# Kernel optimization log

Measured on AMD Instinct MI355X. Metric: run time of the kernel, lower is better.

The kernel has to match this reference:

```python
import jax, jax.numpy as jnp
import numpy as np

N_NODES = 50000
N_EDGES = 800000
IN_DIM = 128
HIDDEN = 32
HEADS = 4
OUT_DIM = 40
NEG_SLOPE = 0.2


def _segment_softmax(logits, seg, num_segments):
    # logits: [E, H], seg: [E] destination node ids
    m = jax.ops.segment_max(logits, seg, num_segments=num_segments)  # [N, H]
    e = jnp.exp(logits - m[seg])
    s = jax.ops.segment_sum(e, seg, num_segments=num_segments)  # [N, H]
    return e / s[seg]


def _gat_conv(x, src, dst, W, a_src, a_dst, b, heads, out_ch, concat):
    N = x.shape[0]
    h = (x @ W).reshape(N, heads, out_ch)  # [N, H, C]
    alpha_src = jnp.einsum('nhc,hc->nh', h, a_src)  # [N, H]
    alpha_dst = jnp.einsum('nhc,hc->nh', h, a_dst)  # [N, H]
    logits = jax.nn.leaky_relu(alpha_src[src] + alpha_dst[dst], NEG_SLOPE)  # [E, H]
    alpha = _segment_softmax(logits, dst, N)  # [E, H]
    msg = h[src] * alpha[:, :, None]  # [E, H, C]
    out = jax.ops.segment_sum(msg, dst, num_segments=N)  # [N, H, C]
    if concat:
        out = out.reshape(N, heads * out_ch)
    else:
        out = out.mean(axis=1)
    return out + b


def setup_inputs() -> dict:
    key = jax.random.key(0)
    ks = jax.random.split(key, 12)
    x = jax.random.normal(ks[0], (N_NODES, IN_DIM), dtype=jnp.float32)
    edge_index = jax.random.randint(ks[1], (2, N_EDGES), 0, N_NODES, dtype=jnp.int64 if jax.config.read('jax_enable_x64') else jnp.int32)
    s1 = 1.0 / np.sqrt(IN_DIM)
    W1 = jax.random.uniform(ks[2], (IN_DIM, HEADS * HIDDEN), jnp.float32, -s1, s1)
    att_src1 = jax.random.uniform(ks[3], (HEADS, HIDDEN), jnp.float32, -1, 1) / np.sqrt(HIDDEN)
    att_dst1 = jax.random.uniform(ks[4], (HEADS, HIDDEN), jnp.float32, -1, 1) / np.sqrt(HIDDEN)
    b1 = jnp.zeros((HEADS * HIDDEN,), jnp.float32)
    s2 = 1.0 / np.sqrt(HEADS * HIDDEN)
    W2 = jax.random.uniform(ks[5], (HEADS * HIDDEN, OUT_DIM), jnp.float32, -s2, s2)
    att_src2 = jax.random.uniform(ks[6], (1, OUT_DIM), jnp.float32, -1, 1) / np.sqrt(OUT_DIM)
    att_dst2 = jax.random.uniform(ks[7], (1, OUT_DIM), jnp.float32, -1, 1) / np.sqrt(OUT_DIM)
    b2 = jnp.zeros((OUT_DIM,), jnp.float32)
    return {
        'x': x, 'edge_index': edge_index,
        'W1': W1, 'att_src1': att_src1, 'att_dst1': att_dst1, 'b1': b1,
        'W2': W2, 'att_src2': att_src2, 'att_dst2': att_dst2, 'b2': b2,
    }


def reference(x, edge_index, W1, att_src1, att_dst1, b1, W2, att_src2, att_dst2, b2):
    N = x.shape[0]
    # PyG GATConv default add_self_loops=True
    loop = jnp.arange(N, dtype=edge_index.dtype)
    src = jnp.concatenate([edge_index[0], loop])
    dst = jnp.concatenate([edge_index[1], loop])
    # dropout(p=0.6) is identity in eval mode
    h = _gat_conv(x, src, dst, W1, att_src1, att_dst1, b1, HEADS, HIDDEN, concat=True)
    h = jax.nn.relu(h)
    out = _gat_conv(h, src, dst, W2, att_src2, att_dst2, b2, 1, OUT_DIM, concat=True)
    return out
```

## Files before the change

### kernel.cpp

```cpp
#include <hip/hip_runtime.h>
#include <hip/hip_bf16.h>
#include <hip/hip_fp16.h>
#include <math.h>

#define N_NODES 50000
#define N_EDGES 800000
#define E_TOT   850000
#define IN_DIM  128
#define HID     32
#define HEADS   4
#define D1      128
#define OUT_DIM 40
#define H2P     64
#define NEG_SLOPE 0.2f
#define CAP     96

#define SCAN_TILE 1024
#define SCAN_NB   ((N_NODES + SCAN_TILE - 1) / SCAN_TILE)
#define GEMM1_NB  ((N_NODES + 63) / 64)
#define W2T_LD    132

typedef _Float16 f16x8 __attribute__((ext_vector_type(8)));
typedef float    f32x4 __attribute__((ext_vector_type(4)));

__global__ __launch_bounds__(256) void init_wf_deg(
    const float* __restrict__ W, _Float16* __restrict__ wf, int* __restrict__ deg)
{
  const int b = blockIdx.x, t = threadIdx.x;
  if (b < 64) {
    int tid = b * 256 + t;
    int j = tid & 7, lane = (tid >> 3) & 63, nt = (tid >> 9) & 7, kc = tid >> 12;
    int k = kc * 32 + ((lane >> 4) << 3) + j;
    int n = nt * 16 + (lane & 15);
    wf[tid] = (_Float16)W[k * D1 + n];
  } else {
    int i = (b - 64) * 256 + t;
    if (i < N_NODES) deg[i] = 0;
  }
}

__global__ __launch_bounds__(256) void gemm1_mfma_count(
    const float* __restrict__ x, const _Float16* __restrict__ wf,
    const float* __restrict__ as_v, const float* __restrict__ ad_v,
    _Float16* __restrict__ h1h, float* __restrict__ asrc, float* __restrict__ adst,
    const int* __restrict__ ei, int* __restrict__ deg)
{
  const int t = threadIdx.x;
  const int wave = t >> 6, lane = t & 63;
  const int lr = lane & 15, lq = lane >> 4;
  const int rowbase = blockIdx.x * 64 + wave * 16;
  const int arow = rowbase + lr;

  f32x4 acc[8];
#pragma unroll
  for (int nt = 0; nt < 8; ++nt) acc[nt] = (f32x4){0.f, 0.f, 0.f, 0.f};

  const float* xrow = x + (size_t)arow * IN_DIM;
  const f16x8* wfv = reinterpret_cast<const f16x8*>(wf);
#pragma unroll
  for (int kc = 0; kc < 4; ++kc) {
    float4 lo = make_float4(0.f, 0.f, 0.f, 0.f), hi = lo;
    if (arow < N_NODES) {
      lo = *reinterpret_cast<const float4*>(xrow + kc * 32 + lq * 8);
      hi = *reinterpret_cast<const float4*>(xrow + kc * 32 + lq * 8 + 4);
    }
    f16x8 a;
    a[0] = (_Float16)lo.x; a[1] = (_Float16)lo.y; a[2] = (_Float16)lo.z; a[3] = (_Float16)lo.w;
    a[4] = (_Float16)hi.x; a[5] = (_Float16)hi.y; a[6] = (_Float16)hi.z; a[7] = (_Float16)hi.w;
    const f16x8* bbase = wfv + (size_t)(kc * 8) * 64 + lane;
#pragma unroll
    for (int nt = 0; nt < 8; ++nt) {
      f16x8 bfrag = bbase[nt * 64];
      acc[nt] = __builtin_amdgcn_mfma_f32_16x16x32_f16(a, bfrag, acc[nt], 0, 0, 0);
    }
  }

  float as_lo[4], as_hi[4], ad_lo[4], ad_hi[4];
#pragma unroll
  for (int h = 0; h < 4; ++h) {
    as_lo[h] = as_v[h * HID + lr];      ad_lo[h] = ad_v[h * HID + lr];
    as_hi[h] = as_v[h * HID + 16 + lr]; ad_hi[h] = ad_v[h * HID + 16 + lr];
  }
#pragma unroll
  for (int nt = 0; nt < 8; ++nt) {
#pragma unroll
    for (int r = 0; r < 4; ++r) {
      int m = rowbase + lq * 4 + r;
      if (m < N_NODES) h1h[(size_t)m * D1 + nt * 16 + lr] = (_Float16)acc[nt][r];
    }
  }
#pragma unroll
  for (int h = 0; h < 4; ++h) {
#pragma unroll
    for (int r = 0; r < 4; ++r) {
      float ps = acc[2 * h][r] * as_lo[h] + acc[2 * h + 1][r] * as_hi[h];
      float pd = acc[2 * h][r] * ad_lo[h] + acc[2 * h + 1][r] * ad_hi[h];
#pragma unroll
      for (int off = 1; off < 16; off <<= 1) {
        ps += __shfl_xor(ps, off, 64);
        pd += __shfl_xor(pd, off, 64);
      }
      int m = rowbase + lq * 4 + r;
      if (lr == 0 && m < N_NODES) {
        asrc[m * HEADS + h] = ps;
        adst[m * HEADS + h] = pd;
      }
    }
  }
  for (int e = blockIdx.x * 256 + t; e < E_TOT; e += gridDim.x * 256) {
    int d = (e < N_EDGES) ? ei[N_EDGES + e] : e - N_EDGES;
    atomicAdd(deg + d, 1);
  }
}

__global__ __launch_bounds__(256) void scan_p1(const int* __restrict__ deg,
                                               int* __restrict__ blocksum)
{
  int base = blockIdx.x * SCAN_TILE + threadIdx.x * 4;
  int s = 0;
#pragma unroll
  for (int i = 0; i < 4; ++i) {
    int idx = base + i;
    if (idx < N_NODES) s += deg[idx];
  }
#pragma unroll
  for (int off = 1; off < 64; off <<= 1) s += __shfl_xor(s, off, 64);
  __shared__ int ws[4];
  if ((threadIdx.x & 63) == 0) ws[threadIdx.x >> 6] = s;
  __syncthreads();
  if (threadIdx.x == 0) blocksum[blockIdx.x] = ws[0] + ws[1] + ws[2] + ws[3];
}

__global__ void scan_p2(const int* __restrict__ blocksum, int* __restrict__ blockoff,
                        int* __restrict__ row_off)
{
  int t = threadIdx.x;
  int v = (t < SCAN_NB) ? blocksum[t] : 0;
  int incl = v;
#pragma unroll
  for (int off = 1; off < 64; off <<= 1) {
    int u = __shfl_up(incl, off, 64);
    if (t >= off) incl += u;
  }
  if (t < SCAN_NB) blockoff[t] = incl - v;
  if (t == 0) row_off[N_NODES] = E_TOT;
}

__global__ __launch_bounds__(256) void scan_p3(const int* __restrict__ deg,
                                               const int* __restrict__ blockoff,
                                               int* __restrict__ row_off,
                                               int* __restrict__ cursor)
{
  const int t = threadIdx.x;
  const int lane = t & 63, wid = t >> 6;
  int base = blockIdx.x * SCAN_TILE + t * 4;
  int local[4]; int lsum = 0;
#pragma unroll
  for (int i = 0; i < 4; ++i) {
    int idx = base + i;
    local[i] = (idx < N_NODES) ? deg[idx] : 0;
    lsum += local[i];
  }
  int incl = lsum;
#pragma unroll
  for (int off = 1; off < 64; off <<= 1) {
    int u = __shfl_up(incl, off, 64);
    if (lane >= off) incl += u;
  }
  __shared__ int wtot[4];
  if (lane == 63) wtot[wid] = incl;
  __syncthreads();
  int wpre = 0;
  for (int w = 0; w < wid; ++w) wpre += wtot[w];
  int run = blockoff[blockIdx.x] + wpre + (incl - lsum);
#pragma unroll
  for (int i = 0; i < 4; ++i) {
    int idx = base + i;
    if (idx < N_NODES) { row_off[idx] = run; cursor[idx] = run; run += local[i]; }
  }
}

__global__ void scatter_csr(const int* __restrict__ ei, int* __restrict__ cursor,
                            int* __restrict__ csr_src)
{
  int e = blockIdx.x * blockDim.x + threadIdx.x;
  if (e >= E_TOT) return;
  int s, d;
  if (e < N_EDGES) { s = ei[e]; d = ei[N_EDGES + e]; }
  else             { s = d = e - N_EDGES; }
  int pos = atomicAdd(cursor + d, 1);
  csr_src[pos] = s;
}

__global__ __launch_bounds__(256) void agg1(
    const int* __restrict__ row_off, const int* __restrict__ csr_src,
    const float* __restrict__ asrc, const float* __restrict__ adst,
    const __half* __restrict__ h1h, const float* __restrict__ b1,
    float* __restrict__ lbuf, float* __restrict__ z)
{
  __shared__ float cbuf[4][CAP * 4];
  const int w = threadIdx.x >> 6;
  int n = blockIdx.x * 4 + w;
  if (n >= N_NODES) return;
  const int lane = threadIdx.x & 63;
  const int start = row_off[n], end = row_off[n + 1];
  const bool useL = (end - start) <= CAP;
  float* cb = cbuf[w];
  const int h = lane & 3;
  const float adst_h = adst[n * HEADS + h];
  float vmax = -1e30f;
  for (int i = start + (lane >> 2); i < end; i += 16)
    vmax = fmaxf(vmax, asrc[csr_src[i] * HEADS + h]);
#pragma unroll
  for (int off = 4; off < 64; off <<= 1)
    vmax = fmaxf(vmax, __shfl_xor(vmax, off, 64));
  float v = vmax + adst_h;
  const float mle = v > 0.f ? v : NEG_SLOPE * v;
  float ssum = 0.f;
  for (int i = start + (lane >> 2); i < end; i += 16) {
    float tv = asrc[csr_src[i] * HEADS + h] + adst_h;
    float le = tv > 0.f ? tv : NEG_SLOPE * tv;
    float e = __expf(le - mle);
    if (useL) cb[(i - start) * 4 + h] = e;
    else      lbuf[(size_t)i * 4 + h] = e;
    ssum += e;
  }
#pragma unroll
  for (int off = 4; off < 64; off <<= 1)
    ssum += __shfl_xor(ssum, off, 64);
  const int hh = lane >> 4;
  const float inv = 1.f / __shfl(ssum, hh, 64);
  float2 acc = make_float2(0.f, 0.f);
  if (useL) {
    int i = start;
    for (; i + 8 <= end; i += 8) {
      float cc[8]; float2 vv[8];
#pragma unroll
      for (int u = 0; u < 8; ++u) {
        int s = csr_src[i + u];
        cc[u] = cb[(i + u - start) * 4 + hh];
        vv[u] = __half22float2(*(reinterpret_cast<const __half2*>(h1h + (size_t)s * D1) + lane));
      }
#pragma unroll
      for (int u = 0; u < 8; ++u) {
        acc.x += cc[u] * vv[u].x;
        acc.y += cc[u] * vv[u].y;
      }
    }
    for (; i < end; ++i) {
      int s = csr_src[i];
      float c = cb[(i - start) * 4 + hh];
      float2 hv = __half22float2(*(reinterpret_cast<const __half2*>(h1h + (size_t)s * D1) + lane));
      acc.x += c * hv.x;
      acc.y += c * hv.y;
    }
  } else {
    for (int i = start; i < end; ++i) {
      int s = csr_src[i];
      float c = lbuf[(size_t)i * 4 + hh];
      float2 hv = __half22float2(*(reinterpret_cast<const __half2*>(h1h + (size_t)s * D1) + lane));
      acc.x += c * hv.x;
      acc.y += c * hv.y;
    }
  }
  float2 bb = *reinterpret_cast<const float2*>(b1 + 2 * lane);
  float r0 = acc.x * inv + bb.x;
  float r1 = acc.y * inv + bb.y;
  float2 o = make_float2(r0 > 0.f ? r0 : 0.f, r1 > 0.f ? r1 : 0.f);
  *reinterpret_cast<float2*>(z + (size_t)n * D1 + 2 * lane) = o;
}

__global__ __launch_bounds__(256) void gemm2(
    const float* __restrict__ z, const float* __restrict__ W2,
    const float* __restrict__ as2, const float* __restrict__ ad2,
    __half* __restrict__ h2h, float* __restrict__ asrc2, float* __restrict__ adst2)
{
  __shared__ float zs[32][IN_DIM];
  __shared__ float w2t[OUT_DIM][W2T_LD];
  const int nb = blockIdx.x * 32;
  const int t  = threadIdx.x;
  for (int i = t; i < 32 * (IN_DIM / 4); i += 256) {
    int r = i >> 5, k4 = (i & 31) * 4;
    int n = nb + r;
    float4 v = (n < N_NODES) ? *reinterpret_cast<const float4*>(z + (size_t)n * IN_DIM + k4)
                             : make_float4(0.f, 0.f, 0.f, 0.f);
    *reinterpret_cast<float4*>(&zs[r][k4]) = v;
  }
  for (int i = t; i < IN_DIM * OUT_DIM; i += 256) {
    int k = i / OUT_DIM, c = i - k * OUT_DIM;
    w2t[c][k] = W2[i];
  }
  __syncthreads();
  const int col = t & 63;
  const int rbase = (t >> 6) * 8;
  const bool valid = col < OUT_DIM;
  const int colc = valid ? col : (OUT_DIM - 1);
  float acc[8];
#pragma unroll
  for (int r = 0; r < 8; ++r) acc[r] = 0.f;
  for (int k = 0; k < IN_DIM; k += 4) {
    float4 wv = *reinterpret_cast<const float4*>(&w2t[colc][k]);
    float4 xv[8];
#pragma unroll
    for (int r = 0; r < 8; ++r)
      xv[r] = *reinterpret_cast<const float4*>(&zs[rbase + r][k]);
#pragma unroll
    for (int r = 0; r < 8; ++r)
      acc[r] += xv[r].x * wv.x + xv[r].y * wv.y + xv[r].z * wv.z + xv[r].w * wv.w;
  }
  const float a_s = valid ? as2[col] : 0.f;
  const float a_d = valid ? ad2[col] : 0.f;
#pragma unroll
  for (int r = 0; r < 8; ++r) {
    int n = nb + rbase + r;
    float cs = acc[r] * a_s, cd = acc[r] * a_d;
#pragma unroll
    for (int off = 32; off >= 1; off >>= 1) {
      cs += __shfl_xor(cs, off, 64);
      cd += __shfl_xor(cd, off, 64);
    }
    if (n < N_NODES) {
      if (valid) h2h[(size_t)n * H2P + col] = __float2half_rn(acc[r]);
      if (col == 0) { asrc2[n] = cs; adst2[n] = cd; }
    }
  }
}

__global__ __launch_bounds__(256) void agg2(
    const int* __restrict__ row_off, const int* __restrict__ csr_src,
    const float* __restrict__ asrc, const float* __restrict__ adst,
    const __half* __restrict__ h2h, const float* __restrict__ b2,
    float* __restrict__ lbuf, float* __restrict__ out)
{
  __shared__ float cbuf[4][CAP];
  const int w = threadIdx.x >> 6;
  int n = blockIdx.x * 4 + w;
  if (n >= N_NODES) return;
  const int lane = threadIdx.x & 63;
  const int start = row_off[n], end = row_off[n + 1];
  const bool useL = (end - start) <= CAP;
  float* cb = cbuf[w];
  const float adstn = adst[n];
  float vmax = -1e30f;
  for (int i = start + lane; i < end; i += 64)
    vmax = fmaxf(vmax, asrc[csr_src[i]]);
#pragma unroll
  for (int off = 1; off < 64; off <<= 1)
    vmax = fmaxf(vmax, __shfl_xor(vmax, off, 64));
  float v = vmax + adstn;
  const float mle = v > 0.f ? v : NEG_SLOPE * v;
  float ssum = 0.f;
  for (int i = start + lane; i < end; i += 64) {
    float t = asrc[csr_src[i]] + adstn;
    float le = t > 0.f ? t : NEG_SLOPE * t;
    float e = __expf(le - mle);
    if (useL) cb[i - start] = e;
    else      lbuf[i] = e;
    ssum += e;
  }
#pragma unroll
  for (int off = 1; off < 64; off <<= 1)
    ssum += __shfl_xor(ssum, off, 64);
  const float inv = 1.f / ssum;
  if (lane < OUT_DIM) {
    float acc = 0.f;
    if (useL) {
      int i = start;
      for (; i + 8 <= end; i += 8) {
        float cc[8]; float vv[8];
#pragma unroll
        for (int u = 0; u < 8; ++u) {
          cc[u] = cb[i + u - start];
          vv[u] = __half2float(h2h[(size_t)csr_src[i + u] * H2P + lane]);
        }
#pragma unroll
        for (int u = 0; u < 8; ++u) acc += cc[u] * vv[u];
      }
      for (; i < end; ++i)
        acc += cb[i - start] * __half2float(h2h[(size_t)csr_src[i] * H2P + lane]);
    } else {
      for (int i = start; i < end; ++i)
        acc += lbuf[i] * __half2float(h2h[(size_t)csr_src[i] * H2P + lane]);
    }
    out[(size_t)n * OUT_DIM + lane] = acc * inv + b2[lane];
  }
}

extern "C" void kernel_launch(void* const* d_in, const int* in_sizes, int n_in,
                              void* d_out, int out_size, void* d_ws, size_t ws_size,
                              hipStream_t stream)
{
  const float* x    = (const float*)d_in[0];
  const int*   ei   = (const int*)  d_in[1];
  const float* W1   = (const float*)d_in[2];
  const float* as1  = (const float*)d_in[3];
  const float* ad1  = (const float*)d_in[4];
  const float* b1   = (const float*)d_in[5];
  const float* W2   = (const float*)d_in[6];
  const float* as2  = (const float*)d_in[7];
  const float* ad2  = (const float*)d_in[8];
  const float* b2   = (const float*)d_in[9];
  float* out = (float*)d_out;

  float* ws = (float*)d_ws;
  _Float16* h1h = (_Float16*)(ws + 0);
  __half*   h2h = (__half*)(ws + 0);
  float* z     = ws +  6400000;
  float* asrc1 = ws + 12800000;
  float* adst1 = ws + 13000000;
  float* asrc2 = ws + 13200000;
  float* adst2 = ws + 13250000;
  int* deg     = (int*)(ws + 13300000);
  int* row_off = (int*)(ws + 13350000);
  int* cursor  = (int*)(ws + 13410000);
  int* csr_src = (int*)(ws + 13460000);
  int* blocksum= (int*)(ws + 14320000);
  int* blockoff= (int*)(ws + 14320100);
  float* lbuf  = ws + 14400000;
  _Float16* wf = (_Float16*)(ws + 17800000);

  const int B = 256;
  init_wf_deg<<<64 + (N_NODES + B - 1) / B, B, 0, stream>>>(W1, wf, deg);
  gemm1_mfma_count<<<GEMM1_NB, B, 0, stream>>>(x, wf, as1, ad1, h1h, asrc1, adst1, ei, deg);
  scan_p1<<<SCAN_NB, B, 0, stream>>>(deg, blocksum);
  scan_p2<<<1, 64, 0, stream>>>(blocksum, blockoff, row_off);
  scan_p3<<<SCAN_NB, B, 0, stream>>>(deg, blockoff, row_off, cursor);
  scatter_csr<<<(E_TOT + B - 1) / B, B, 0, stream>>>(ei, cursor, csr_src);
  agg1<<<(N_NODES + 3) / 4, B, 0, stream>>>(row_off, csr_src, asrc1, adst1,
                                            (const __half*)h1h, b1, lbuf, z);
  gemm2<<<(N_NODES + 31) / 32, B, 0, stream>>>(z, W2, as2, ad2, h2h, asrc2, adst2);
  agg2<<<(N_NODES + 3) / 4, B, 0, stream>>>(row_off, csr_src, asrc2, adst2, h2h, b2, lbuf, out);
}
```

Measured before the change: 319.2 us.

## Fuse CSR scatter into GEMM1 launch and store CSR sources as 16-bit

Degree counting moves out of the GEMM1 kernel into its own kernel that runs before the scan. The CSR scatter is then merged into the GEMM1 launch as extra blocks, so the scatter and the dense GEMM can run concurrently. CSR source indices are stored as unsigned short to halve gather-index traffic in agg1 and agg2. This is only valid because node ids fit in 16 bits (N_NODES=50000), so it depends on this problem size.

Measured after the change: 310.4 us. 1.03x faster.

```diff
diff --git a/kernel.cpp b/kernel.cpp
--- a/kernel.cpp
+++ b/kernel.cpp
@@ -18,6 +18,7 @@
 #define SCAN_TILE 1024
 #define SCAN_NB   ((N_NODES + SCAN_TILE - 1) / SCAN_TILE)
 #define GEMM1_NB  ((N_NODES + 63) / 64)
+#define SCT_NB    ((E_TOT + 255) / 256)
 #define W2T_LD    132
 
 typedef _Float16 f16x8 __attribute__((ext_vector_type(8)));
@@ -39,13 +40,100 @@
   }
 }
 
-__global__ __launch_bounds__(256) void gemm1_mfma_count(
+__global__ void count_deg(const int* __restrict__ ei, int* __restrict__ deg)
+{
+  int e = blockIdx.x * blockDim.x + threadIdx.x;
+  if (e >= E_TOT) return;
+  int d = (e < N_EDGES) ? ei[N_EDGES + e] : e - N_EDGES;
+  atomicAdd(deg + d, 1);
+}
+
+__global__ __launch_bounds__(256) void scan_p1(const int* __restrict__ deg,
+                                               int* __restrict__ blocksum)
+{
+  int base = blockIdx.x * SCAN_TILE + threadIdx.x * 4;
+  int s = 0;
+#pragma unroll
+  for (int i = 0; i < 4; ++i) {
+    int idx = base + i;
+    if (idx < N_NODES) s += deg[idx];
+  }
+#pragma unroll
+  for (int off = 1; off < 64; off <<= 1) s += __shfl_xor(s, off, 64);
+  __shared__ int ws[4];
+  if ((threadIdx.x & 63) == 0) ws[threadIdx.x >> 6] = s;
+  __syncthreads();
+  if (threadIdx.x == 0) blocksum[blockIdx.x] = ws[0] + ws[1] + ws[2] + ws[3];
+}
+
+__global__ void scan_p2(const int* __restrict__ blocksum, int* __restrict__ blockoff,
+                        int* __restrict__ row_off)
+{
+  int t = threadIdx.x;
+  int v = (t < SCAN_NB) ? blocksum[t] : 0;
+  int incl = v;
+#pragma unroll
+  for (int off = 1; off < 64; off <<= 1) {
+    int u = __shfl_up(incl, off, 64);
+    if (t >= off) incl += u;
+  }
+  if (t < SCAN_NB) blockoff[t] = incl - v;
+  if (t == 0) row_off[N_NODES] = E_TOT;
+}
+
+__global__ __launch_bounds__(256) void scan_p3(const int* __restrict__ deg,
+                                               const int* __restrict__ blockoff,
+                                               int* __restrict__ row_off,
+                                               int* __restrict__ cursor)
+{
+  const int t = threadIdx.x;
+  const int lane = t & 63, wid = t >> 6;
+  int base = blockIdx.x * SCAN_TILE + t * 4;
+  int local[4]; int lsum = 0;
+#pragma unroll
+  for (int i = 0; i < 4; ++i) {
+    int idx = base + i;
+    local[i] = (idx < N_NODES) ? deg[idx] : 0;
+    lsum += local[i];
+  }
+  int incl = lsum;
+#pragma unroll
+  for (int off = 1; off < 64; off <<= 1) {
+    int u = __shfl_up(incl, off, 64);
+    if (lane >= off) incl += u;
+  }
+  __shared__ int wtot[4];
+  if (lane == 63) wtot[wid] = incl;
+  __syncthreads();
+  int wpre = 0;
+  for (int w = 0; w < wid; ++w) wpre += wtot[w];
+  int run = blockoff[blockIdx.x] + wpre + (incl - lsum);
+#pragma unroll
+  for (int i = 0; i < 4; ++i) {
+    int idx = base + i;
+    if (idx < N_NODES) { row_off[idx] = run; cursor[idx] = run; run += local[i]; }
+  }
+}
+
+__global__ __launch_bounds__(256) void gemm1_mfma_scatter(
     const float* __restrict__ x, const _Float16* __restrict__ wf,
     const float* __restrict__ as_v, const float* __restrict__ ad_v,
     _Float16* __restrict__ h1h, float* __restrict__ asrc, float* __restrict__ adst,
-    const int* __restrict__ ei, int* __restrict__ deg)
+    const int* __restrict__ ei, int* __restrict__ cursor,
+    unsigned short* __restrict__ csr_src)
 {
   const int t = threadIdx.x;
+  if (blockIdx.x >= GEMM1_NB) {
+    int e = (blockIdx.x - GEMM1_NB) * 256 + t;
+    if (e < E_TOT) {
+      int s, d;
+      if (e < N_EDGES) { s = ei[e]; d = ei[N_EDGES + e]; }
+      else             { s = d = e - N_EDGES; }
+      int pos = atomicAdd(cursor + d, 1);
+      csr_src[pos] = (unsigned short)s;
+    }
+    return;
+  }
   const int wave = t >> 6, lane = t & 63;
   const int lr = lane & 15, lq = lane >> 4;
   const int rowbase = blockIdx.x * 64 + wave * 16;
@@ -107,93 +195,10 @@
       }
     }
   }
-  for (int e = blockIdx.x * 256 + t; e < E_TOT; e += gridDim.x * 256) {
-    int d = (e < N_EDGES) ? ei[N_EDGES + e] : e - N_EDGES;
-    atomicAdd(deg + d, 1);
-  }
-}
-
-__global__ __launch_bounds__(256) void scan_p1(const int* __restrict__ deg,
-                                               int* __restrict__ blocksum)
-{
-  int base = blockIdx.x * SCAN_TILE + threadIdx.x * 4;
-  int s = 0;
-#pragma unroll
-  for (int i = 0; i < 4; ++i) {
-    int idx = base + i;
-    if (idx < N_NODES) s += deg[idx];
-  }
-#pragma unroll
-  for (int off = 1; off < 64; off <<= 1) s += __shfl_xor(s, off, 64);
-  __shared__ int ws[4];
-  if ((threadIdx.x & 63) == 0) ws[threadIdx.x >> 6] = s;
-  __syncthreads();
-  if (threadIdx.x == 0) blocksum[blockIdx.x] = ws[0] + ws[1] + ws[2] + ws[3];
-}
-
-__global__ void scan_p2(const int* __restrict__ blocksum, int* __restrict__ blockoff,
-                        int* __restrict__ row_off)
-{
-  int t = threadIdx.x;
-  int v = (t < SCAN_NB) ? blocksum[t] : 0;
-  int incl = v;
-#pragma unroll
-  for (int off = 1; off < 64; off <<= 1) {
-    int u = __shfl_up(incl, off, 64);
-    if (t >= off) incl += u;
-  }
-  if (t < SCAN_NB) blockoff[t] = incl - v;
-  if (t == 0) row_off[N_NODES] = E_TOT;
-}
-
-__global__ __launch_bounds__(256) void scan_p3(const int* __restrict__ deg,
-                                               const int* __restrict__ blockoff,
-                                               int* __restrict__ row_off,
-                                               int* __restrict__ cursor)
-{
-  const int t = threadIdx.x;
-  const int lane = t & 63, wid = t >> 6;
-  int base = blockIdx.x * SCAN_TILE + t * 4;
-  int local[4]; int lsum = 0;
-#pragma unroll
-  for (int i = 0; i < 4; ++i) {
-    int idx = base + i;
-    local[i] = (idx < N_NODES) ? deg[idx] : 0;
-    lsum += local[i];
-  }
-  int incl = lsum;
-#pragma unroll
-  for (int off = 1; off < 64; off <<= 1) {
-    int u = __shfl_up(incl, off, 64);
-    if (lane >= off) incl += u;
-  }
-  __shared__ int wtot[4];
-  if (lane == 63) wtot[wid] = incl;
-  __syncthreads();
-  int wpre = 0;
-  for (int w = 0; w < wid; ++w) wpre += wtot[w];
-  int run = blockoff[blockIdx.x] + wpre + (incl - lsum);
-#pragma unroll
-  for (int i = 0; i < 4; ++i) {
-    int idx = base + i;
-    if (idx < N_NODES) { row_off[idx] = run; cursor[idx] = run; run += local[i]; }
-  }
-}
-
-__global__ void scatter_csr(const int* __restrict__ ei, int* __restrict__ cursor,
-                            int* __restrict__ csr_src)
-{
-  int e = blockIdx.x * blockDim.x + threadIdx.x;
-  if (e >= E_TOT) return;
-  int s, d;
-  if (e < N_EDGES) { s = ei[e]; d = ei[N_EDGES + e]; }
-  else             { s = d = e - N_EDGES; }
-  int pos = atomicAdd(cursor + d, 1);
-  csr_src[pos] = s;
 }
 
 __global__ __launch_bounds__(256) void agg1(
-    const int* __restrict__ row_off, const int* __restrict__ csr_src,
+    const int* __restrict__ row_off, const unsigned short* __restrict__ csr_src,
     const float* __restrict__ asrc, const float* __restrict__ adst,
     const __half* __restrict__ h1h, const float* __restrict__ b1,
     float* __restrict__ lbuf, float* __restrict__ z)
@@ -210,7 +215,7 @@
   const float adst_h = adst[n * HEADS + h];
   float vmax = -1e30f;
   for (int i = start + (lane >> 2); i < end; i += 16)
-    vmax = fmaxf(vmax, asrc[csr_src[i] * HEADS + h]);
+    vmax = fmaxf(vmax, asrc[(int)csr_src[i] * HEADS + h]);
 #pragma unroll
   for (int off = 4; off < 64; off <<= 1)
     vmax = fmaxf(vmax, __shfl_xor(vmax, off, 64));
@@ -218,7 +223,7 @@
   const float mle = v > 0.f ? v : NEG_SLOPE * v;
   float ssum = 0.f;
   for (int i = start + (lane >> 2); i < end; i += 16) {
-    float tv = asrc[csr_src[i] * HEADS + h] + adst_h;
+    float tv = asrc[(int)csr_src[i] * HEADS + h] + adst_h;
     float le = tv > 0.f ? tv : NEG_SLOPE * tv;
     float e = __expf(le - mle);
     if (useL) cb[(i - start) * 4 + h] = e;
@@ -327,7 +332,7 @@
 }
 
 __global__ __launch_bounds__(256) void agg2(
-    const int* __restrict__ row_off, const int* __restrict__ csr_src,
+    const int* __restrict__ row_off, const unsigned short* __restrict__ csr_src,
     const float* __restrict__ asrc, const float* __restrict__ adst,
     const __half* __restrict__ h2h, const float* __restrict__ b2,
     float* __restrict__ lbuf, float* __restrict__ out)
@@ -413,7 +418,7 @@
   int* deg     = (int*)(ws + 13300000);
   int* row_off = (int*)(ws + 13350000);
   int* cursor  = (int*)(ws + 13410000);
-  int* csr_src = (int*)(ws + 13460000);
+  unsigned short* csr_src = (unsigned short*)(ws + 13460000);
   int* blocksum= (int*)(ws + 14320000);
   int* blockoff= (int*)(ws + 14320100);
   float* lbuf  = ws + 14400000;
@@ -421,11 +426,12 @@
 
   const int B = 256;
   init_wf_deg<<<64 + (N_NODES + B - 1) / B, B, 0, stream>>>(W1, wf, deg);
-  gemm1_mfma_count<<<GEMM1_NB, B, 0, stream>>>(x, wf, as1, ad1, h1h, asrc1, adst1, ei, deg);
+  count_deg<<<SCT_NB, B, 0, stream>>>(ei, deg);
   scan_p1<<<SCAN_NB, B, 0, stream>>>(deg, blocksum);
   scan_p2<<<1, 64, 0, stream>>>(blocksum, blockoff, row_off);
   scan_p3<<<SCAN_NB, B, 0, stream>>>(deg, blockoff, row_off, cursor);
-  scatter_csr<<<(E_TOT + B - 1) / B, B, 0, stream>>>(ei, cursor, csr_src);
+  gemm1_mfma_scatter<<<GEMM1_NB + SCT_NB, B, 0, stream>>>(
+      x, wf, as1, ad1, h1h, asrc1, adst1, ei, cursor, csr_src);
   agg1<<<(N_NODES + 3) / 4, B, 0, stream>>>(row_off, csr_src, asrc1, adst1,
                                             (const __half*)h1h, b1, lbuf, z);
   gemm2<<<(N_NODES + 31) / 32, B, 0, stream>>>(z, W2, as2, ad2, h2h, asrc2, adst2);
```
